# Performance work log

Measured on AMD Instinct MI355X. Metric: run time of the kernel, lower is better.

## Reference

```python
import jax, jax.numpy as jnp
import numpy as np

N_HEADS = 16
DIM = 1024
BS, SLEN = 2, 2048
EPS = 1e-12  # F.normalize eps


def setup_inputs() -> dict:
    key = jax.random.key(0)
    ks = jax.random.split(key, 10)
    d = DIM
    inp = {
        "x": jax.random.normal(ks[0], (BS, SLEN, d), dtype=jnp.float32),
        # causal attention mask, as produced by get_masks(causal=True)
        "mask": jnp.tril(jnp.ones((SLEN, SLEN), dtype=bool))[None].repeat(BS, axis=0),
        "Wq": jax.random.normal(ks[1], (d, d), dtype=jnp.float32) / np.sqrt(d),
        "bq": jax.random.normal(ks[2], (d,), dtype=jnp.float32) * 0.02,
        "Wk": jax.random.normal(ks[3], (d, d), dtype=jnp.float32) / np.sqrt(d),
        "bk": jax.random.normal(ks[4], (d,), dtype=jnp.float32) * 0.02,
        "Wv": jax.random.normal(ks[5], (d, d), dtype=jnp.float32) / np.sqrt(d),
        "bv": jax.random.normal(ks[6], (d,), dtype=jnp.float32) * 0.02,
        "Wo": jax.random.normal(ks[7], (d, d), dtype=jnp.float32) / np.sqrt(d),
        "bo": jax.random.normal(ks[8], (d,), dtype=jnp.float32) * 0.02,
        # learnable scale for normalized (cosine) attention
        "attention_scale": jnp.ones((1,), dtype=jnp.float32) / np.sqrt(d // N_HEADS),
    }
    return inp


def _shape(t, bs, h, dph):
    # (bs, len, dim) -> (bs, h, len, dph)
    return t.reshape(bs, -1, h, dph).transpose(0, 2, 1, 3)


def reference(x, mask, Wq, bq, Wk, bk, Wv, bv, Wo, bo, attention_scale):
    bs, qlen, dim = x.shape
    h = N_HEADS
    dph = dim // h

    q = _shape(x @ Wq + bq, bs, h, dph)  # (bs, h, qlen, dph)
    k = _shape(x @ Wk + bk, bs, h, dph)
    v = _shape(x @ Wv + bv, bs, h, dph)

    # normalized (cosine) attention: L2-normalize q and k, learned scale
    q = q / jnp.maximum(jnp.linalg.norm(q, axis=-1, keepdims=True), EPS)
    k = k / jnp.maximum(jnp.linalg.norm(k, axis=-1, keepdims=True), EPS)
    q = q * attention_scale

    scores = jnp.einsum("bhqd,bhkd->bhqk", q, k)  # (bs, h, qlen, klen)
    scores = jnp.where(mask[:, None, :, :], scores, -jnp.inf)
    weights = jax.nn.softmax(scores, axis=-1)

    ctx = jnp.einsum("bhqk,bhkd->bhqd", weights, v)
    ctx = ctx.transpose(0, 2, 1, 3).reshape(bs, qlen, dim)
    return ctx @ Wo + bo
```

## Files before the change

kernel.cpp:

```cpp
#include <hip/hip_runtime.h>
#include <math.h>

#define NH 16
#define DPH 64
#define SLEN 2048
#define BSZ 2
#define DIM 1024
#define NTOK (BSZ * SLEN)
#define LOG2E 1.44269504088896f

typedef unsigned short ushortT;
typedef __attribute__((ext_vector_type(8))) short short8;
typedef __attribute__((ext_vector_type(4))) float f32x4;

typedef __attribute__((address_space(1))) const unsigned int gu32c;
typedef __attribute__((address_space(3))) unsigned int lu32;

__device__ __forceinline__ void gld16(const void* g, void* l) {
    __builtin_amdgcn_global_load_lds((gu32c*)g, (lu32*)l, 16, 0, 0);
}

__device__ __forceinline__ ushortT f2bf(float f) {
    unsigned int u = __builtin_bit_cast(unsigned int, f);
    u = u + 0x7fffu + ((u >> 16) & 1u);
    return (ushortT)(u >> 16);
}

__device__ __forceinline__ unsigned int cvtpk_bf16(float a, float b) {
    unsigned int r;
    asm("v_cvt_pk_bf16_f32 %0, %1, %2" : "=v"(r) : "v"(a), "v"(b));
    return r;
}

__global__ __launch_bounds__(256) void cvt_all(const float* __restrict__ x,
                                               ushortT* __restrict__ xb,
                                               const float* __restrict__ W0, const float* __restrict__ W1,
                                               const float* __restrict__ W2, const float* __restrict__ W3,
                                               ushortT* __restrict__ T0, ushortT* __restrict__ T1,
                                               ushortT* __restrict__ T2, ushortT* __restrict__ T3) {
    __shared__ float tile[64][65];
    const int tid = threadIdx.x;
    const int bid = blockIdx.x;
    if (bid < 2048) {
        size_t i = (size_t)bid * 256 + tid;
        float4 a = *(const float4*)&x[i * 8];
        float4 b = *(const float4*)&x[i * 8 + 4];
        short8 v;
        v[0] = (short)f2bf(a.x); v[1] = (short)f2bf(a.y);
        v[2] = (short)f2bf(a.z); v[3] = (short)f2bf(a.w);
        v[4] = (short)f2bf(b.x); v[5] = (short)f2bf(b.y);
        v[6] = (short)f2bf(b.z); v[7] = (short)f2bf(b.w);
        *(short8*)&xb[i * 8] = v;
        return;
    }
    const int widx = bid - 2048;
    const int z = widx >> 8, rem = widx & 255;
    const float* W = z == 0 ? W0 : z == 1 ? W1 : z == 2 ? W2 : W3;
    ushortT* T = z == 0 ? T0 : z == 1 ? T1 : z == 2 ? T2 : T3;
    const int kb = (rem >> 4) * 64, nb = (rem & 15) * 64;
#pragma unroll
    for (int it = 0; it < 4; it++) {
        int chunk = it * 256 + tid;
        int r = chunk >> 4, c4 = (chunk & 15) * 4;
        *(float4*)&tile[r][c4] = *(const float4*)&W[(size_t)(kb + r) * DIM + nb + c4];
    }
    __syncthreads();
#pragma unroll
    for (int it = 0; it < 2; it++) {
        int chunk = it * 256 + tid;
        int n = chunk >> 3, k8 = (chunk & 7) * 8;
        short8 o;
#pragma unroll
        for (int j = 0; j < 8; j++) o[j] = (short)f2bf(tile[k8 + j][n]);
        *(short8*)&T[(size_t)(nb + n) * DIM + kb + k8] = o;
    }
}

__global__ __launch_bounds__(512, 2) void gemm_qkv8(const ushortT* __restrict__ A,
                                                    const ushortT* __restrict__ Bt,
                                                    const float* __restrict__ bq,
                                                    const float* __restrict__ bk,
                                                    const float* __restrict__ bv,
                                                    const float* __restrict__ ascale,
                                                    ushortT* __restrict__ Qb,
                                                    ushortT* __restrict__ Kb,
                                                    ushortT* __restrict__ VF) {
    __shared__ __align__(16) ushortT lds[65536];
    const int tid = threadIdx.x;
    const int lane = tid & 63, wid = tid >> 6;
    const int wm = wid >> 2, wn = wid & 3;
    const int lo = lane & 15, hi = lane >> 4;
    const int bid = blockIdx.x;
    const int swz = (bid & 7) * 24 + (bid >> 3);
    const int bx = swz % 12, by = swz / 12;
    const int row0 = by * 256, col0 = bx * 256;
    const int srow2 = tid >> 2, sc = tid & 3;
    f32x4 acc[8][4] = {};
    short8 af[8], bfr[4];

    auto stage = [&](int isA, int buf, int ksh, int kt) {
        const ushortT* g = isA ? A : Bt;
        int r0 = isA ? row0 : col0;
        int base = (isA ? 0 : 32768) + (buf * 2 + ksh) * 8192;
#pragma unroll
        for (int r = 0; r < 2; r++) {
            int rl = r * 128 + srow2;
            int gch = sc ^ ((rl >> 1) & 3);
            gld16(&g[(size_t)(r0 + rl) * DIM + kt * 64 + ksh * 32 + gch * 8],
                  &lds[base + r * 4096 + tid * 8]);
        }
    };
    auto loadA8 = [&](int buf, int ks) {
        int base = (buf * 2 + ks) * 8192;
#pragma unroll
        for (int mm = 0; mm < 8; mm++) {
            int row = wm * 128 + mm * 16 + lo;
            af[mm] = *(const short8*)&lds[base + row * 32 + (hi ^ ((row >> 1) & 3)) * 8];
        }
    };
    auto loadB = [&](int buf, int ks) {
        int base = 32768 + (buf * 2 + ks) * 8192;
#pragma unroll
        for (int n = 0; n < 4; n++) {
            int row = wn * 64 + n * 16 + lo;
            bfr[n] = *(const short8*)&lds[base + row * 32 + (hi ^ ((row >> 1) & 3)) * 8];
        }
    };
    auto mfma32 = [&]() {
        __builtin_amdgcn_s_setprio(1);
#pragma unroll
        for (int mm = 0; mm < 8; mm++)
#pragma unroll
            for (int n = 0; n < 4; n++)
                acc[mm][n] = __builtin_amdgcn_mfma_f32_16x16x32_bf16(
                    af[mm], bfr[n], acc[mm][n], 0, 0, 0);
        __builtin_amdgcn_s_setprio(0);
    };

    stage(0, 0, 0, 0); stage(1, 0, 0, 0);
    stage(0, 0, 1, 0); stage(1, 0, 1, 0);

#pragma unroll 1
    for (int t = 0; t < 16; ++t) {
        const int cur = t & 1, nxt = cur ^ 1;
        const bool more = (t < 15);
        asm volatile("s_waitcnt vmcnt(4)" ::: "memory");
        asm volatile("s_barrier" ::: "memory");
        loadA8(cur, 0); loadB(cur, 0);
        if (more) { stage(0, nxt, 0, t + 1); stage(1, nxt, 0, t + 1); }
        mfma32();
        if (more) { asm volatile("s_waitcnt vmcnt(4)" ::: "memory"); }
        else      { asm volatile("s_waitcnt vmcnt(0)" ::: "memory"); }
        asm volatile("s_barrier" ::: "memory");
        loadA8(cur, 1); loadB(cur, 1);
        if (more) { stage(0, nxt, 1, t + 1); stage(1, nxt, 1, t + 1); }
        mfma32();
    }
    __syncthreads();

    const int cg = col0 + wn * 64;
    const int which = cg >> 10;
    const int cwin = cg & 1023;
    const int h = cwin >> 6;
    const int t0g = row0 + wm * 128;
    const int b = t0g >> 11, tok0 = t0g & (SLEN - 1);
    const float* bias = which == 0 ? bq : which == 1 ? bk : bv;

    float bb4[4];
#pragma unroll
    for (int n = 0; n < 4; n++) bb4[n] = bias[cwin + n * 16 + lo];
#pragma unroll
    for (int m = 0; m < 8; m++)
#pragma unroll
        for (int n = 0; n < 4; n++)
#pragma unroll
            for (int r = 0; r < 4; r++) acc[m][n][r] += bb4[n];

    if (which < 2) {
        float asc = (which == 0) ? ascale[0] * LOG2E : 1.0f;
#pragma unroll
        for (int m = 0; m < 8; m++)
#pragma unroll
            for (int r = 0; r < 4; r++) {
                float ss = acc[m][0][r] * acc[m][0][r] + acc[m][1][r] * acc[m][1][r] +
                           acc[m][2][r] * acc[m][2][r] + acc[m][3][r] * acc[m][3][r];
#pragma unroll
                for (int o = 8; o > 0; o >>= 1) ss += __shfl_xor(ss, o);
                float sc2 = asc / fmaxf(sqrtf(ss), 1e-12f);
#pragma unroll
                for (int n = 0; n < 4; n++) acc[m][n][r] *= sc2;
            }
    }

    ushortT* tl = &lds[wid * 8192];
    if (which < 2) {
#pragma unroll
        for (int m = 0; m < 8; m++)
#pragma unroll
            for (int n = 0; n < 4; n++)
#pragma unroll
                for (int r = 0; r < 4; r++) {
                    int row = m * 16 + 4 * hi + r;
                    int c = n * 2 + (lo >> 3);
                    tl[row * 64 + ((c ^ (row & 7)) << 3) + (lo & 7)] = f2bf(acc[m][n][r]);
                }
        ushortT* op = which == 0 ? Qb : Kb;
        const size_t base = ((size_t)(b * NH + h) * SLEN + tok0) * DPH;
#pragma unroll
        for (int j = 0; j < 16; j++) {
            int cid = j * 64 + lane;
            int rowL = cid >> 3, c = cid & 7;
            uint4 v = *(const uint4*)&tl[rowL * 64 + ((c ^ (rowL & 7)) << 3)];
            *(uint4*)&op[base + (size_t)cid * 8] = v;
        }
    } else {
#pragma unroll
        for (int m = 0; m < 8; m++)
#pragma unroll
            for (int n = 0; n < 4; n++)
#pragma unroll
                for (int r = 0; r < 4; r++) {
                    int row = m * 16 + 4 * hi + r;
                    int c = n * 2 + (lo >> 3);
                    tl[row * 64 + ((c ^ ((row >> 3) & 7)) << 3) + (lo & 7)] = f2bf(acc[m][n][r]);
                }
        const int bh = b * NH + h;
        const int kt0 = tok0 >> 6;
#pragma unroll
        for (int i = 0; i < 16; i++) {
            int kk = i >> 3;
            int c = i & 7;
            int jd = c >> 1, ks2 = c & 1;
            int colL = jd * 16 + lo;
            int c2 = colL >> 3;
            short8 v;
#pragma unroll
            for (int e = 0; e < 8; e++) {
                int rowL = kk * 64 + ks2 * 32 + 8 * hi + e;
                v[e] = (short)tl[rowL * 64 + ((c2 ^ ((rowL >> 3) & 7)) << 3) + (colL & 7)];
            }
            *(short8*)&VF[((size_t)bh * 32 + kt0 + kk) * 4096 + (size_t)(c * 64 + lane) * 8] = v;
        }
    }
}

__global__ __launch_bounds__(512, 2) void gemm_oproj(const ushortT* __restrict__ A,
                                                     const ushortT* __restrict__ Bt,
                                                     const float* __restrict__ bias,
                                                     float* __restrict__ outF) {
    __shared__ __align__(16) ushortT lds[32768];
    const int tid = threadIdx.x;
    const int lane = tid & 63, wid = tid >> 6;
    const int wm = wid >> 2, wn = wid & 3;
    const int lo = lane & 15, hi = lane >> 4;
    const int bid = blockIdx.x;
    const int swz = (bid & 7) * 32 + (bid >> 3);
    const int bx = swz & 7, by = swz >> 3;
    const int row0 = by * 128, col0 = bx * 128;
    const int srow = tid >> 2, sc = tid & 3;
    f32x4 acc[4][2] = {};
    short8 afO[2], bfO[2];

    auto stage = [&](int isA, int buf, int ksh, int kt) {
        const ushortT* g = isA ? A : Bt;
        int r0 = isA ? row0 : col0;
        int base = (isA ? 0 : 16384) + (buf * 2 + ksh) * 4096;
        int gch = sc ^ ((srow >> 1) & 3);
        gld16(&g[(size_t)(r0 + srow) * DIM + kt * 64 + ksh * 32 + gch * 8],
              &lds[base + tid * 8]);
    };
    auto loadAO = [&](int buf, int ks, int mh) {
        int base = (buf * 2 + ks) * 4096;
#pragma unroll
        for (int mm = 0; mm < 2; mm++) {
            int row = wm * 64 + (mh * 2 + mm) * 16 + lo;
            afO[mm] = *(const short8*)&lds[base + row * 32 + (hi ^ ((row >> 1) & 3)) * 8];
        }
    };
    auto loadBO = [&](int buf, int ks) {
        int base = 16384 + (buf * 2 + ks) * 4096;
#pragma unroll
        for (int n = 0; n < 2; n++) {
            int row = wn * 32 + n * 16 + lo;
            bfO[n] = *(const short8*)&lds[base + row * 32 + (hi ^ ((row >> 1) & 3)) * 8];
        }
    };
    auto mfma4 = [&](int mh) {
        __builtin_amdgcn_s_setprio(1);
#pragma unroll
        for (int mm = 0; mm < 2; mm++)
#pragma unroll
            for (int n = 0; n < 2; n++)
                acc[mh * 2 + mm][n] = __builtin_amdgcn_mfma_f32_16x16x32_bf16(
                    afO[mm], bfO[n], acc[mh * 2 + mm][n], 0, 0, 0);
        __builtin_amdgcn_s_setprio(0);
    };

    stage(1, 0, 0, 0); stage(0, 0, 0, 0);
    stage(1, 0, 1, 0); stage(0, 0, 1, 0);
    stage(1, 1, 0, 1); stage(0, 1, 0, 1);

#pragma unroll 1
    for (int it = 0; it < 8; ++it) {
        const int o = it * 2 + 1;
        const bool more = (it < 7);
        asm volatile("s_waitcnt vmcnt(4)" ::: "memory");
        asm volatile("s_barrier" ::: "memory");
        loadAO(0, 0, 0); loadBO(0, 0);
        stage(1, 1, 1, o);
        mfma4(0);
        asm volatile("s_barrier" ::: "memory");
        loadAO(0, 0, 1);
        stage(0, 1, 1, o);
        mfma4(1);
        asm volatile("s_waitcnt vmcnt(4)" ::: "memory");
        asm volatile("s_barrier" ::: "memory");
        loadAO(0, 1, 0); loadBO(0, 1);
        if (more) stage(1, 0, 0, o + 1);
        mfma4(0);
        asm volatile("s_barrier" ::: "memory");
        loadAO(0, 1, 1);
        if (more) stage(0, 0, 0, o + 1);
        mfma4(1);
        if (more) { asm volatile("s_waitcnt vmcnt(4)" ::: "memory"); }
        else      { asm volatile("s_waitcnt vmcnt(2)" ::: "memory"); }
        asm volatile("s_barrier" ::: "memory");
        loadAO(1, 0, 0); loadBO(1, 0);
        if (more) stage(1, 0, 1, o + 1);
        mfma4(0);
        asm volatile("s_barrier" ::: "memory");
        loadAO(1, 0, 1);
        if (more) stage(0, 0, 1, o + 1);
        mfma4(1);
        if (more) { asm volatile("s_waitcnt vmcnt(4)" ::: "memory"); }
        else      { asm volatile("s_waitcnt vmcnt(0)" ::: "memory"); }
        asm volatile("s_barrier" ::: "memory");
        loadAO(1, 1, 0); loadBO(1, 1);
        if (more) stage(1, 1, 0, o + 2);
        mfma4(0);
        asm volatile("s_barrier" ::: "memory");
        loadAO(1, 1, 1);
        if (more) stage(0, 1, 0, o + 2);
        mfma4(1);
    }
    __syncthreads();

    float bb[2];
#pragma unroll
    for (int n = 0; n < 2; n++) bb[n] = bias[col0 + wn * 32 + n * 16 + lo];
#pragma unroll
    for (int m = 0; m < 4; m++)
#pragma unroll
        for (int n = 0; n < 2; n++)
#pragma unroll
            for (int r = 0; r < 4; r++) acc[m][n][r] += bb[n];

    float* tl = (float*)&lds[wid * 4096];
#pragma unroll
    for (int m = 0; m < 4; m++)
#pragma unroll
        for (int n = 0; n < 2; n++)
#pragma unroll
            for (int r = 0; r < 4; r++) {
                int row = m * 16 + hi * 4 + r;
                int col = n * 16 + lo;
                int cc = col >> 2;
                tl[row * 32 + ((cc ^ (row & 7)) << 2) + (col & 3)] = acc[m][n][r];
            }
#pragma unroll
    for (int j = 0; j < 8; j++) {
        int cid = j * 64 + lane;
        int rowR = cid >> 3, cc = cid & 7;
        f32x4 v = *(const f32x4*)&tl[rowR * 32 + ((cc ^ (rowR & 7)) << 2)];
        int rg = row0 + wm * 64 + rowR;
        int cgl = col0 + wn * 32 + cc * 4;
        *(f32x4*)&outF[(size_t)rg * DIM + cgl] = v;
    }
}

__global__ __launch_bounds__(512, 4) void attn(const ushortT* __restrict__ Q,
                                               const ushortT* __restrict__ K,
                                               const ushortT* __restrict__ VF,
                                               const float* __restrict__ scale,
                                               ushortT* __restrict__ ctx) {
    __shared__ __align__(16) ushortT Ks[2][2][64 * 64];
    __shared__ __align__(16) ushortT Ps[8 * 16 * 64];
    const int tid = threadIdx.x, lane = tid & 63, wid = tid >> 6;
    const int wg = wid & 3, sg = wid >> 2;
    const int bh = blockIdx.x, p = blockIdx.y;
    const int qt = sg ? p : 31 - p;
    const int kbmax = 31 - p;
    const size_t hb = (size_t)bh * SLEN * DPH;
    const int lo = lane & 15, hi = lane >> 4;
    const float mshift = fabsf(scale[0]) * LOG2E;

    short8 aq[2];
    {
        const int qrow = qt * 64 + wg * 16 + lo;
#pragma unroll
        for (int ks = 0; ks < 2; ks++)
            aq[ks] = *(const short8*)&Q[hb + (size_t)qrow * DPH + ks * 32 + 8 * hi];
    }

    const int srow = tid >> 3, sslot = tid & 7;
    const int sldsoff = srow * 64 + ((sslot ^ (srow & 7)) << 3);
    {
        uint4 k0 = *(const uint4*)&K[hb + (size_t)srow * DPH + sslot * 8];
        uint4 k1 = *(const uint4*)&K[hb + (size_t)(64 + srow) * DPH + sslot * 8];
        *(uint4*)&Ks[0][0][sldsoff] = k0;
        *(uint4*)&Ks[0][1][sldsoff] = k1;
    }
    __syncthreads();

    f32x4 accd[4] = {};
    float lp = 0.f;

    for (int rd = 0; rd * 2 <= kbmax; ++rd) {
        const int cur = rd & 1;
        const int tn0 = 2 * rd + 2, tn1 = 2 * rd + 3;
        const bool h0 = tn0 <= kbmax, h1 = tn1 <= kbmax;
        uint4 n0, n1;
        if (h0) n0 = *(const uint4*)&K[hb + (size_t)(tn0 * 64 + srow) * DPH + sslot * 8];
        if (h1) n1 = *(const uint4*)&K[hb + (size_t)(tn1 * 64 + srow) * DPH + sslot * 8];

#pragma unroll
        for (int sub = 0; sub < 2; ++sub) {
            const int kb = 2 * rd + sub;
            if (kb <= qt) {
                short8 bv[8];
                const ushortT* vt = &VF[(((size_t)bh * 32 + kb) * 512 + lane) * 8];
#pragma unroll
                for (int c = 0; c < 8; c++) bv[c] = *(const short8*)&vt[(size_t)c * 512];

                f32x4 sf[4] = {};
                __builtin_amdgcn_s_setprio(1);
#pragma unroll
                for (int ks = 0; ks < 2; ks++)
#pragma unroll
                    for (int j = 0; j < 4; j++) {
                        int row = j * 16 + lo;
                        short8 bk = *(const short8*)&Ks[cur][sub][row * 64 + (((ks * 4 + hi) ^ (row & 7)) << 3)];
                        sf[j] = __builtin_amdgcn_mfma_f32_16x16x32_bf16(bk, aq[ks], sf[j], 0, 0, 0);
                    }
                __builtin_amdgcn_s_setprio(0);

                if (kb == qt) {
#pragma unroll
                    for (int j = 0; j < 4; j++)
#pragma unroll
                        for (int r = 0; r < 4; r++)
                            if (j * 16 + 4 * hi + r > wg * 16 + lo) sf[j][r] = -INFINITY;
                }

#pragma unroll
                for (int j = 0; j < 4; j++) {
                    float pv0 = __builtin_amdgcn_exp2f(sf[j][0] - mshift);
                    float pv1 = __builtin_amdgcn_exp2f(sf[j][1] - mshift);
                    float pv2 = __builtin_amdgcn_exp2f(sf[j][2] - mshift);
                    float pv3 = __builtin_amdgcn_exp2f(sf[j][3] - mshift);
                    lp += (pv0 + pv1) + (pv2 + pv3);
                    uint2 pk;
                    pk.x = cvtpk_bf16(pv0, pv1);
                    pk.y = cvtpk_bf16(pv2, pv3);
                    int slot = (4 * j + hi) ^ (2 * (lo & 7));
                    *(uint2*)&Ps[wid * 1024 + lo * 64 + slot * 4] = pk;
                }

                __builtin_amdgcn_s_setprio(1);
#pragma unroll
                for (int ks = 0; ks < 2; ks++) {
                    int slot0 = (8 * ks + 2 * hi) ^ (2 * (lo & 7));
                    short8 ap = *(const short8*)&Ps[wid * 1024 + lo * 64 + slot0 * 4];
#pragma unroll
                    for (int jd = 0; jd < 4; jd++)
                        accd[jd] = __builtin_amdgcn_mfma_f32_16x16x32_bf16(ap, bv[jd * 2 + ks], accd[jd], 0, 0, 0);
                }
                __builtin_amdgcn_s_setprio(0);
            }
        }

        if (h0) *(uint4*)&Ks[cur ^ 1][0][sldsoff] = n0;
        if (h1) *(uint4*)&Ks[cur ^ 1][1][sldsoff] = n1;
        __syncthreads();
    }

    lp += __shfl_xor(lp, 16);
    lp += __shfl_xor(lp, 32);

    const int b = bh >> 4, h = bh & 15;
#pragma unroll
    for (int r = 0; r < 4; r++) {
        float lr = __shfl(lp, (lane & 48) | (4 * hi + r));
        float inv = 1.0f / lr;
        int t = qt * 64 + wg * 16 + 4 * hi + r;
#pragma unroll
        for (int jd = 0; jd < 4; jd++) {
            int d = jd * 16 + lo;
            ctx[(size_t)(b * SLEN + t) * DIM + h * 64 + d] = f2bf(accd[jd][r] * inv);
        }
    }
}

extern "C" void kernel_launch(void* const* d_in, const int* in_sizes, int n_in,
                              void* d_out, int out_size, void* d_ws,
                              size_t ws_size, hipStream_t stream) {
    const float* x = (const float*)d_in[0];
    const float* Wq = (const float*)d_in[2];
    const float* bq = (const float*)d_in[3];
    const float* Wk = (const float*)d_in[4];
    const float* bk = (const float*)d_in[5];
    const float* Wv = (const float*)d_in[6];
    const float* bv = (const float*)d_in[7];
    const float* Wo = (const float*)d_in[8];
    const float* bo = (const float*)d_in[9];
    const float* ascale = (const float*)d_in[10];
    float* outF = (float*)d_out;

    unsigned char* ws = (unsigned char*)d_ws;
    const size_t MB = 1u << 20;
    ushortT* xb = (ushortT*)(ws);
    ushortT* Wqkvt = (ushortT*)(ws + 8 * MB);
    ushortT* Wot = (ushortT*)(ws + 14 * MB);
    ushortT* Qb = (ushortT*)(ws + 16 * MB);
    ushortT* Kb = (ushortT*)(ws + 24 * MB);
    ushortT* VFb = (ushortT*)(ws + 32 * MB);
    ushortT* ctxb = (ushortT*)(ws + 40 * MB);

    cvt_all<<<3072, 256, 0, stream>>>(x, xb, Wq, Wk, Wv, Wo, Wqkvt,
                                      Wqkvt + (size_t)1024 * 1024,
                                      Wqkvt + (size_t)2048 * 1024, Wot);

    gemm_qkv8<<<dim3(192), 512, 0, stream>>>(xb, Wqkvt, bq, bk, bv, ascale, Qb, Kb, VFb);

    attn<<<dim3(32, 16), 512, 0, stream>>>(Qb, Kb, VFb, ascale, ctxb);

    gemm_oproj<<<dim3(256), 512, 0, stream>>>(ctxb, Wot, bo, outF);
}
```

Before: 95.64 us.

## Use 1024-thread QKV GEMM with smaller per-wave tiles; single-block K staging in attention

The QKV GEMM now runs 16 waves per 256x256 block, each computing a 64x64 sub-tile instead of 128x64. That halves per-wave accumulators and fragments and loads one 16-byte chunk per thread per stage, with the V-fragment epilogue adjusted to match. The attention kernel drops its two-key-blocks-per-round scheme for a simple one-block double buffer, which halves K LDS but doubles the number of barriers. The aggressive launch-bounds hint (1024, 4) may force tight register limits and spilling, and more waves per block also add barrier cost.

```diff
diff --git a/kernel.cpp b/kernel.cpp
--- a/kernel.cpp
+++ b/kernel.cpp
@@ -76,15 +76,15 @@
     }
 }
 
-__global__ __launch_bounds__(512, 2) void gemm_qkv8(const ushortT* __restrict__ A,
-                                                    const ushortT* __restrict__ Bt,
-                                                    const float* __restrict__ bq,
-                                                    const float* __restrict__ bk,
-                                                    const float* __restrict__ bv,
-                                                    const float* __restrict__ ascale,
-                                                    ushortT* __restrict__ Qb,
-                                                    ushortT* __restrict__ Kb,
-                                                    ushortT* __restrict__ VF) {
+__global__ __launch_bounds__(1024, 4) void gemm_qkv8(const ushortT* __restrict__ A,
+                                                     const ushortT* __restrict__ Bt,
+                                                     const float* __restrict__ bq,
+                                                     const float* __restrict__ bk,
+                                                     const float* __restrict__ bv,
+                                                     const float* __restrict__ ascale,
+                                                     ushortT* __restrict__ Qb,
+                                                     ushortT* __restrict__ Kb,
+                                                     ushortT* __restrict__ VF) {
     __shared__ __align__(16) ushortT lds[65536];
     const int tid = threadIdx.x;
     const int lane = tid & 63, wid = tid >> 6;
@@ -94,27 +94,23 @@
     const int swz = (bid & 7) * 24 + (bid >> 3);
     const int bx = swz % 12, by = swz / 12;
     const int row0 = by * 256, col0 = bx * 256;
-    const int srow2 = tid >> 2, sc = tid & 3;
-    f32x4 acc[8][4] = {};
-    short8 af[8], bfr[4];
+    const int srow = tid >> 2, sc = tid & 3;
+    f32x4 acc[4][4] = {};
+    short8 af[4], bfr[4];
 
     auto stage = [&](int isA, int buf, int ksh, int kt) {
         const ushortT* g = isA ? A : Bt;
         int r0 = isA ? row0 : col0;
         int base = (isA ? 0 : 32768) + (buf * 2 + ksh) * 8192;
-#pragma unroll
-        for (int r = 0; r < 2; r++) {
-            int rl = r * 128 + srow2;
-            int gch = sc ^ ((rl >> 1) & 3);
-            gld16(&g[(size_t)(r0 + rl) * DIM + kt * 64 + ksh * 32 + gch * 8],
-                  &lds[base + r * 4096 + tid * 8]);
-        }
-    };
-    auto loadA8 = [&](int buf, int ks) {
+        int gch = sc ^ ((srow >> 1) & 3);
+        gld16(&g[(size_t)(r0 + srow) * DIM + kt * 64 + ksh * 32 + gch * 8],
+              &lds[base + tid * 8]);
+    };
+    auto loadA = [&](int buf, int ks) {
         int base = (buf * 2 + ks) * 8192;
 #pragma unroll
-        for (int mm = 0; mm < 8; mm++) {
-            int row = wm * 128 + mm * 16 + lo;
+        for (int mm = 0; mm < 4; mm++) {
+            int row = wm * 64 + mm * 16 + lo;
             af[mm] = *(const short8*)&lds[base + row * 32 + (hi ^ ((row >> 1) & 3)) * 8];
         }
     };
@@ -126,10 +122,10 @@
             bfr[n] = *(const short8*)&lds[base + row * 32 + (hi ^ ((row >> 1) & 3)) * 8];
         }
     };
-    auto mfma32 = [&]() {
+    auto mfma16 = [&]() {
         __builtin_amdgcn_s_setprio(1);
 #pragma unroll
-        for (int mm = 0; mm < 8; mm++)
+        for (int mm = 0; mm < 4; mm++)
 #pragma unroll
             for (int n = 0; n < 4; n++)
                 acc[mm][n] = __builtin_amdgcn_mfma_f32_16x16x32_bf16(
@@ -144,17 +140,17 @@
     for (int t = 0; t < 16; ++t) {
         const int cur = t & 1, nxt = cur ^ 1;
         const bool more = (t < 15);
-        asm volatile("s_waitcnt vmcnt(4)" ::: "memory");
-        asm volatile("s_barrier" ::: "memory");
-        loadA8(cur, 0); loadB(cur, 0);
+        asm volatile("s_waitcnt vmcnt(2)" ::: "memory");
+        asm volatile("s_barrier" ::: "memory");
+        loadA(cur, 0); loadB(cur, 0);
         if (more) { stage(0, nxt, 0, t + 1); stage(1, nxt, 0, t + 1); }
-        mfma32();
-        if (more) { asm volatile("s_waitcnt vmcnt(4)" ::: "memory"); }
+        mfma16();
+        if (more) { asm volatile("s_waitcnt vmcnt(2)" ::: "memory"); }
         else      { asm volatile("s_waitcnt vmcnt(0)" ::: "memory"); }
         asm volatile("s_barrier" ::: "memory");
-        loadA8(cur, 1); loadB(cur, 1);
+        loadA(cur, 1); loadB(cur, 1);
         if (more) { stage(0, nxt, 1, t + 1); stage(1, nxt, 1, t + 1); }
-        mfma32();
+        mfma16();
     }
     __syncthreads();
 
@@ -162,7 +158,7 @@
     const int which = cg >> 10;
     const int cwin = cg & 1023;
     const int h = cwin >> 6;
-    const int t0g = row0 + wm * 128;
+    const int t0g = row0 + wm * 64;
     const int b = t0g >> 11, tok0 = t0g & (SLEN - 1);
     const float* bias = which == 0 ? bq : which == 1 ? bk : bv;
 
@@ -170,7 +166,7 @@
 #pragma unroll
     for (int n = 0; n < 4; n++) bb4[n] = bias[cwin + n * 16 + lo];
 #pragma unroll
-    for (int m = 0; m < 8; m++)
+    for (int m = 0; m < 4; m++)
 #pragma unroll
         for (int n = 0; n < 4; n++)
 #pragma unroll
@@ -179,7 +175,7 @@
     if (which < 2) {
         float asc = (which == 0) ? ascale[0] * LOG2E : 1.0f;
 #pragma unroll
-        for (int m = 0; m < 8; m++)
+        for (int m = 0; m < 4; m++)
 #pragma unroll
             for (int r = 0; r < 4; r++) {
                 float ss = acc[m][0][r] * acc[m][0][r] + acc[m][1][r] * acc[m][1][r] +
@@ -192,10 +188,10 @@
             }
     }
 
-    ushortT* tl = &lds[wid * 8192];
+    ushortT* tl = &lds[wid * 4096];
     if (which < 2) {
 #pragma unroll
-        for (int m = 0; m < 8; m++)
+        for (int m = 0; m < 4; m++)
 #pragma unroll
             for (int n = 0; n < 4; n++)
 #pragma unroll
@@ -207,7 +203,7 @@
         ushortT* op = which == 0 ? Qb : Kb;
         const size_t base = ((size_t)(b * NH + h) * SLEN + tok0) * DPH;
 #pragma unroll
-        for (int j = 0; j < 16; j++) {
+        for (int j = 0; j < 8; j++) {
             int cid = j * 64 + lane;
             int rowL = cid >> 3, c = cid & 7;
             uint4 v = *(const uint4*)&tl[rowL * 64 + ((c ^ (rowL & 7)) << 3)];
@@ -215,7 +211,7 @@
         }
     } else {
 #pragma unroll
-        for (int m = 0; m < 8; m++)
+        for (int m = 0; m < 4; m++)
 #pragma unroll
             for (int n = 0; n < 4; n++)
 #pragma unroll
@@ -225,21 +221,19 @@
                     tl[row * 64 + ((c ^ ((row >> 3) & 7)) << 3) + (lo & 7)] = f2bf(acc[m][n][r]);
                 }
         const int bh = b * NH + h;
-        const int kt0 = tok0 >> 6;
-#pragma unroll
-        for (int i = 0; i < 16; i++) {
-            int kk = i >> 3;
-            int c = i & 7;
-            int jd = c >> 1, ks2 = c & 1;
+        const int kt = tok0 >> 6;
+#pragma unroll
+        for (int c2i = 0; c2i < 8; c2i++) {
+            int jd = c2i >> 1, ks2 = c2i & 1;
             int colL = jd * 16 + lo;
-            int c2 = colL >> 3;
+            int cc2 = colL >> 3;
             short8 v;
 #pragma unroll
             for (int e = 0; e < 8; e++) {
-                int rowL = kk * 64 + ks2 * 32 + 8 * hi + e;
-                v[e] = (short)tl[rowL * 64 + ((c2 ^ ((rowL >> 3) & 7)) << 3) + (colL & 7)];
+                int rowL = ks2 * 32 + 8 * hi + e;
+                v[e] = (short)tl[rowL * 64 + ((cc2 ^ ((rowL >> 3) & 7)) << 3) + (colL & 7)];
             }
-            *(short8*)&VF[((size_t)bh * 32 + kt0 + kk) * 4096 + (size_t)(c * 64 + lane) * 8] = v;
+            *(short8*)&VF[((size_t)bh * 32 + kt) * 4096 + (size_t)(c2i * 64 + lane) * 8] = v;
         }
     }
 }
@@ -383,7 +377,7 @@
                                                const ushortT* __restrict__ VF,
                                                const float* __restrict__ scale,
                                                ushortT* __restrict__ ctx) {
-    __shared__ __align__(16) ushortT Ks[2][2][64 * 64];
+    __shared__ __align__(16) ushortT Ks[2][64 * 64];
     __shared__ __align__(16) ushortT Ps[8 * 16 * 64];
     const int tid = threadIdx.x, lane = tid & 63, wid = tid >> 6;
     const int wg = wid & 3, sg = wid >> 2;
@@ -404,83 +398,71 @@
 
     const int srow = tid >> 3, sslot = tid & 7;
     const int sldsoff = srow * 64 + ((sslot ^ (srow & 7)) << 3);
-    {
-        uint4 k0 = *(const uint4*)&K[hb + (size_t)srow * DPH + sslot * 8];
-        uint4 k1 = *(const uint4*)&K[hb + (size_t)(64 + srow) * DPH + sslot * 8];
-        *(uint4*)&Ks[0][0][sldsoff] = k0;
-        *(uint4*)&Ks[0][1][sldsoff] = k1;
-    }
+    uint4 kr = *(const uint4*)&K[hb + (size_t)srow * DPH + sslot * 8];
+    *(uint4*)&Ks[0][sldsoff] = kr;
     __syncthreads();
 
     f32x4 accd[4] = {};
     float lp = 0.f;
 
-    for (int rd = 0; rd * 2 <= kbmax; ++rd) {
-        const int cur = rd & 1;
-        const int tn0 = 2 * rd + 2, tn1 = 2 * rd + 3;
-        const bool h0 = tn0 <= kbmax, h1 = tn1 <= kbmax;
-        uint4 n0, n1;
-        if (h0) n0 = *(const uint4*)&K[hb + (size_t)(tn0 * 64 + srow) * DPH + sslot * 8];
-        if (h1) n1 = *(const uint4*)&K[hb + (size_t)(tn1 * 64 + srow) * DPH + sslot * 8];
-
-#pragma unroll
-        for (int sub = 0; sub < 2; ++sub) {
-            const int kb = 2 * rd + sub;
-            if (kb <= qt) {
-                short8 bv[8];
-                const ushortT* vt = &VF[(((size_t)bh * 32 + kb) * 512 + lane) * 8];
-#pragma unroll
-                for (int c = 0; c < 8; c++) bv[c] = *(const short8*)&vt[(size_t)c * 512];
-
-                f32x4 sf[4] = {};
-                __builtin_amdgcn_s_setprio(1);
-#pragma unroll
-                for (int ks = 0; ks < 2; ks++)
-#pragma unroll
-                    for (int j = 0; j < 4; j++) {
-                        int row = j * 16 + lo;
-                        short8 bk = *(const short8*)&Ks[cur][sub][row * 64 + (((ks * 4 + hi) ^ (row & 7)) << 3)];
-                        sf[j] = __builtin_amdgcn_mfma_f32_16x16x32_bf16(bk, aq[ks], sf[j], 0, 0, 0);
-                    }
-                __builtin_amdgcn_s_setprio(0);
-
-                if (kb == qt) {
-#pragma unroll
-                    for (int j = 0; j < 4; j++)
-#pragma unroll
-                        for (int r = 0; r < 4; r++)
-                            if (j * 16 + 4 * hi + r > wg * 16 + lo) sf[j][r] = -INFINITY;
+    for (int kb = 0; kb <= kbmax; kb++) {
+        const int cur = kb & 1;
+        if (kb < kbmax)
+            kr = *(const uint4*)&K[hb + (size_t)((kb + 1) * 64 + srow) * DPH + sslot * 8];
+
+        if (kb <= qt) {
+            short8 bv[8];
+            const ushortT* vt = &VF[(((size_t)bh * 32 + kb) * 512 + lane) * 8];
+#pragma unroll
+            for (int c = 0; c < 8; c++) bv[c] = *(const short8*)&vt[(size_t)c * 512];
+
+            f32x4 sf[4] = {};
+            __builtin_amdgcn_s_setprio(1);
+#pragma unroll
+            for (int ks = 0; ks < 2; ks++)
+#pragma unroll
+                for (int j = 0; j < 4; j++) {
+                    int row = j * 16 + lo;
+                    short8 bk = *(const short8*)&Ks[cur][row * 64 + (((ks * 4 + hi) ^ (row & 7)) << 3)];
+                    sf[j] = __builtin_amdgcn_mfma_f32_16x16x32_bf16(bk, aq[ks], sf[j], 0, 0, 0);
                 }
-
-#pragma unroll
-                for (int j = 0; j < 4; j++) {
-                    float pv0 = __builtin_amdgcn_exp2f(sf[j][0] - mshift);
-                    float pv1 = __builtin_amdgcn_exp2f(sf[j][1] - mshift);
-                    float pv2 = __builtin_amdgcn_exp2f(sf[j][2] - mshift);
-                    float pv3 = __builtin_amdgcn_exp2f(sf[j][3] - mshift);
-                    lp += (pv0 + pv1) + (pv2 + pv3);
-                    uint2 pk;
-                    pk.x = cvtpk_bf16(pv0, pv1);
-                    pk.y = cvtpk_bf16(pv2, pv3);
-                    int slot = (4 * j + hi) ^ (2 * (lo & 7));
-                    *(uint2*)&Ps[wid * 1024 + lo * 64 + slot * 4] = pk;
-                }
-
-                __builtin_amdgcn_s_setprio(1);
-#pragma unroll
-                for (int ks = 0; ks < 2; ks++) {
-                    int slot0 = (8 * ks + 2 * hi) ^ (2 * (lo & 7));
-                    short8 ap = *(const short8*)&Ps[wid * 1024 + lo * 64 + slot0 * 4];
-#pragma unroll
-                    for (int jd = 0; jd < 4; jd++)
-                        accd[jd] = __builtin_amdgcn_mfma_f32_16x16x32_bf16(ap, bv[jd * 2 + ks], accd[jd], 0, 0, 0);
-                }
-                __builtin_amdgcn_s_setprio(0);
+            __builtin_amdgcn_s_setprio(0);
+
+            if (kb == qt) {
+#pragma unroll
+                for (int j = 0; j < 4; j++)
+#pragma unroll
+                    for (int r = 0; r < 4; r++)
+                        if (j * 16 + 4 * hi + r > wg * 16 + lo) sf[j][r] = -INFINITY;
             }
-        }
-
-        if (h0) *(uint4*)&Ks[cur ^ 1][0][sldsoff] = n0;
-        if (h1) *(uint4*)&Ks[cur ^ 1][1][sldsoff] = n1;
+
+#pragma unroll
+            for (int j = 0; j < 4; j++) {
+                float pv0 = __builtin_amdgcn_exp2f(sf[j][0] - mshift);
+                float pv1 = __builtin_amdgcn_exp2f(sf[j][1] - mshift);
+                float pv2 = __builtin_amdgcn_exp2f(sf[j][2] - mshift);
+                float pv3 = __builtin_amdgcn_exp2f(sf[j][3] - mshift);
+                lp += (pv0 + pv1) + (pv2 + pv3);
+                uint2 pk;
+                pk.x = cvtpk_bf16(pv0, pv1);
+                pk.y = cvtpk_bf16(pv2, pv3);
+                int slot = (4 * j + hi) ^ (2 * (lo & 7));
+                *(uint2*)&Ps[wid * 1024 + lo * 64 + slot * 4] = pk;
+            }
+
+            __builtin_amdgcn_s_setprio(1);
+#pragma unroll
+            for (int ks = 0; ks < 2; ks++) {
+                int slot0 = (8 * ks + 2 * hi) ^ (2 * (lo & 7));
+                short8 ap = *(const short8*)&Ps[wid * 1024 + lo * 64 + slot0 * 4];
+#pragma unroll
+                for (int jd = 0; jd < 4; jd++)
+                    accd[jd] = __builtin_amdgcn_mfma_f32_16x16x32_bf16(ap, bv[jd * 2 + ks], accd[jd], 0, 0, 0);
+            }
+            __builtin_amdgcn_s_setprio(0);
+        }
+
+        if (kb < kbmax) *(uint4*)&Ks[cur ^ 1][sldsoff] = kr;
         __syncthreads();
     }
 
@@ -530,7 +512,7 @@
                                       Wqkvt + (size_t)1024 * 1024,
                                       Wqkvt + (size_t)2048 * 1024, Wot);
 
-    gemm_qkv8<<<dim3(192), 512, 0, stream>>>(xb, Wqkvt, bq, bk, bv, ascale, Qb, Kb, VFb);
+    gemm_qkv8<<<dim3(192), 1024, 0, stream>>>(xb, Wqkvt, bq, bk, bv, ascale, Qb, Kb, VFb);
 
     attn<<<dim3(32, 16), 512, 0, stream>>>(Qb, Kb, VFb, ascale, ctxb);
 
```

Result: faster. 91.61 us (-4.2%).
